# Kernel optimization log

Measured on AMD Instinct MI355X. Metric: run time of the kernel, lower is better.

The kernel has to match this reference:

```python
import jax, jax.numpy as jnp
import numpy as np

CATE_BIN = (512, 128, 256, 256, 64, 256, 256, 16, 256)
NUM_BIN = (64, 16, 128, 64, 128, 64, 512, 512)
TABLE_SIZES = CATE_BIN + NUM_BIN  # 17 tables
EMB_DIM = 16
MAX_ROWS = max(TABLE_SIZES)  # 512; tables padded/stacked for a fused gather
HIDDEN = [256, 256, 128]
OUT = 1
BATCH = 262144
BN_EPS = 1e-5


def setup_inputs() -> dict:
    key = jax.random.key(0)
    ks = jax.random.split(key, 32)
    # indices: per-column cardinality
    cols = [jax.random.randint(jax.random.fold_in(ks[0], i), (BATCH,), 0, n, dtype=jnp.int32)
            for i, n in enumerate(TABLE_SIZES)]
    x = jnp.stack(cols, axis=1)  # [B, 17] int32
    # fused/padded embedding tables: [17, MAX_ROWS, EMB_DIM]
    tables = jax.random.normal(ks[1], (len(TABLE_SIZES), MAX_ROWS, EMB_DIM), dtype=jnp.float32) * 0.05
    d_in = len(TABLE_SIZES) * EMB_DIM  # 272
    dims = [d_in] + HIDDEN
    params = {}
    for i in range(len(HIDDEN)):
        params[f"W{i}"] = jax.random.normal(ks[2 + 4 * i], (dims[i], dims[i + 1]), dtype=jnp.float32) * (1.0 / np.sqrt(dims[i]))
        params[f"b{i}"] = jnp.zeros((dims[i + 1],), dtype=jnp.float32)
        params[f"g{i}"] = jnp.ones((dims[i + 1],), dtype=jnp.float32)
        params[f"be{i}"] = jnp.zeros((dims[i + 1],), dtype=jnp.float32)
    params["Wout"] = jax.random.normal(ks[30], (HIDDEN[-1], OUT), dtype=jnp.float32) * (1.0 / np.sqrt(HIDDEN[-1]))
    params["bout"] = jnp.zeros((OUT,), dtype=jnp.float32)
    return {"x": x, "tables": tables, **params}


def _batchnorm(h, g, b):
    mu = jnp.mean(h, axis=0)
    var = jnp.var(h, axis=0)  # biased, matching torch BN forward
    return g * (h - mu) * jax.lax.rsqrt(var + BN_EPS) + b


def reference(x, tables, W0, b0, g0, be0, W1, b1, g1, be1, W2, b2, g2, be2, Wout, bout):
    # fused table-batched gather: [B, 17, 16] -> [B, 272]
    emb = tables[jnp.arange(tables.shape[0]), x]  # [B, 17, E]
    h = emb.reshape(emb.shape[0], -1)
    for W, b, g, be in ((W0, b0, g0, be0), (W1, b1, g1, be1), (W2, b2, g2, be2)):
        h = jax.nn.relu(h @ W + b)
        h = _batchnorm(h, g, be)
    return h @ Wout + bout
```

## Files before the change

### kernel.cpp

```cpp
#include <hip/hip_runtime.h>
#include <stdint.h>

#define BR 262144
#define NTAB 17
#define MAXR 512
#define DIN 272
#define AS0 296
#define ASM 264
#define NCOPY 32
#define BNEPS 1e-5f

typedef __attribute__((ext_vector_type(8))) short short8;
typedef __attribute__((ext_vector_type(4))) float f32x4;
typedef __attribute__((ext_vector_type(4))) unsigned short ushort4w;

__device__ __forceinline__ unsigned short f2bf(float f) {
  union { float f; unsigned u; } v; v.f = f;
  return (unsigned short)((v.u + 0x7FFFu + ((v.u >> 16) & 1u)) >> 16);
}
__device__ __forceinline__ float bf2f(unsigned short h) {
  union { unsigned u; float f; } v; v.u = ((unsigned)h) << 16;
  return v.f;
}

__global__ void k_prep0(const float* __restrict__ W0, const float* __restrict__ tables,
                        unsigned short* __restrict__ pW0, unsigned short* __restrict__ tb,
                        float* __restrict__ stats) {
  int tid = blockIdx.x * blockDim.x + threadIdx.x;
  int nth = gridDim.x * blockDim.x;
  for (int i = tid; i < NCOPY * 1280; i += nth) stats[i] = 0.f;
  for (int e = tid; e < 17408; e += nth) {
    const float* src = tables + (size_t)e * 8;
    f32x4 v0 = ((const f32x4*)src)[0];
    f32x4 v1 = ((const f32x4*)src)[1];
    unsigned short tmp[8];
#pragma unroll
    for (int j = 0; j < 4; j++) { tmp[j] = f2bf(v0[j]); tmp[4 + j] = f2bf(v1[j]); }
    *(short8*)&tb[(size_t)e * 8] = *(short8*)tmp;
  }
  for (int e = tid; e < 9 * 16 * 64; e += nth) {
    int l = e & 63, f = e >> 6;
    int nf = f & 15, ks = f >> 4;
    int col = nf * 16 + (l & 15);
    int kb = ks * 32 + ((l >> 4) << 3);
    unsigned short tmp[8];
#pragma unroll
    for (int j = 0; j < 8; j++) {
      int k = kb + j;
      tmp[j] = f2bf(k < DIN ? W0[k * 256 + col] : 0.f);
    }
    *(short8*)&pW0[(size_t)e * 8] = *(short8*)tmp;
  }
}

template <int KP, int NP>
__global__ void k_fold(const float* __restrict__ stats, int offSum, int offSq,
                       const float* __restrict__ g, const float* __restrict__ be,
                       const float* __restrict__ W, const float* __restrict__ b,
                       unsigned short* __restrict__ pW, float* __restrict__ bOut) {
  __shared__ float sa[KP], sc[KP];
  int tid = threadIdx.x;
  if (tid < KP) {
    float s = 0.f, q = 0.f;
    for (int c = 0; c < NCOPY; c++) {
      s += stats[c * 1280 + offSum + tid];
      q += stats[c * 1280 + offSq + tid];
    }
    float mu = s * (1.f / BR);
    float var = fmaxf(q * (1.f / BR) - mu * mu, 0.f);
    float a = g[tid] * rsqrtf(var + BNEPS);
    sa[tid] = a;
    sc[tid] = be[tid] - mu * a;
  }
  __syncthreads();
  const int NFT = NP / 16;
  const int ENT = (KP / 32) * NFT * 64;
  for (int e = blockIdx.x * blockDim.x + tid; e < ENT; e += gridDim.x * blockDim.x) {
    int l = e & 63, f = e >> 6;
    int nf = f % NFT, ks = f / NFT;
    int col = nf * 16 + (l & 15);
    int kb = ks * 32 + ((l >> 4) << 3);
    unsigned short tmp[8];
#pragma unroll
    for (int j = 0; j < 8; j++) {
      int k = kb + j;
      tmp[j] = f2bf(sa[k] * W[k * NP + col]);
    }
    *(short8*)&pW[(size_t)e * 8] = *(short8*)tmp;
  }
  if (blockIdx.x == 0 && tid < NP) {
    float s = b[tid];
    for (int k = 0; k < KP; k++) s += sc[k] * W[k * NP + tid];
    bOut[tid] = s;
  }
}

__global__ void k_foldout(const float* __restrict__ stats, int offSum, int offSq,
                          const float* __restrict__ g, const float* __restrict__ be,
                          const float* __restrict__ Wout, const float* __restrict__ bout,
                          float* __restrict__ woutp, float* __restrict__ boutp) {
  __shared__ float red[128];
  int tid = threadIdx.x;
  float s = 0.f, q = 0.f;
  for (int c = 0; c < NCOPY; c++) {
    s += stats[c * 1280 + offSum + tid];
    q += stats[c * 1280 + offSq + tid];
  }
  float mu = s * (1.f / BR);
  float var = fmaxf(q * (1.f / BR) - mu * mu, 0.f);
  float a = g[tid] * rsqrtf(var + BNEPS);
  float c = be[tid] - mu * a;
  float w = Wout[tid];
  woutp[tid] = a * w;
  red[tid] = c * w;
  __syncthreads();
  for (int st = 64; st > 0; st >>= 1) {
    if (tid < st) red[tid] += red[tid + st];
    __syncthreads();
  }
  if (tid == 0) boutp[0] = red[0] + bout[0];
}

template <int KSTEPS, int N, int AST, int MF>
__device__ __forceinline__ void gemm_body(unsigned short* As, const unsigned short* __restrict__ pW,
                                          const float* __restrict__ bias, unsigned short* __restrict__ Y,
                                          int brow, float* ssum, float* ssq,
                                          float* __restrict__ gsum, float* __restrict__ gsq) {
  const int tid = threadIdx.x;
  const int lane = tid & 63, wave = tid >> 6;
  constexpr int WC = N / 64;
  const int wc = wave % WC, wr = wave / WC;
  const int wrow = wr * (MF * 16);
  const int wcolf = wc * 4;
  const int arow = lane & 15;
  const int koff = (lane >> 4) << 3;
  const int grp = lane >> 4;

  f32x4 zero4 = {0.f, 0.f, 0.f, 0.f};
  f32x4 acc[MF][4];
#pragma unroll
  for (int mf = 0; mf < MF; mf++)
#pragma unroll
    for (int nf = 0; nf < 4; nf++) acc[mf][nf] = zero4;

  short8 bcur[4], bnxt[4];
#pragma unroll
  for (int nf = 0; nf < 4; nf++)
    bcur[nf] = *(const short8*)&pW[(size_t)((wcolf + nf) * 64 + lane) * 8];

#pragma unroll
  for (int ks = 0; ks < KSTEPS; ks++) {
    if (ks + 1 < KSTEPS) {
#pragma unroll
      for (int nf = 0; nf < 4; nf++)
        bnxt[nf] = *(const short8*)&pW[(size_t)(((ks + 1) * (N / 16) + wcolf + nf) * 64 + lane) * 8];
    }
#pragma unroll
    for (int mf = 0; mf < MF; mf++) {
      short8 am = *(const short8*)&As[(wrow + mf * 16 + arow) * AST + ks * 32 + koff];
#pragma unroll
      for (int nf = 0; nf < 4; nf++)
        acc[mf][nf] = __builtin_amdgcn_mfma_f32_16x16x32_bf16(bcur[nf], am, acc[mf][nf], 0, 0, 0);
    }
#pragma unroll
    for (int nf = 0; nf < 4; nf++) bcur[nf] = bnxt[nf];
  }

  __syncthreads();

#pragma unroll
  for (int nf = 0; nf < 4; nf++) {
    const int c0 = (wcolf + nf) * 16 + grp * 4;
    f32x4 bb = *(const f32x4*)&bias[c0];
    float s[4] = {0.f, 0.f, 0.f, 0.f}, q[4] = {0.f, 0.f, 0.f, 0.f};
#pragma unroll
    for (int mf = 0; mf < MF; mf++) {
      const int r = wrow + mf * 16 + arow;
      unsigned short o[4];
#pragma unroll
      for (int j = 0; j < 4; j++) {
        float v = fmaxf(acc[mf][nf][j] + bb[j], 0.f);
        o[j] = f2bf(v);
        s[j] += v;
        q[j] += v * v;
      }
      *(ushort4w*)&As[r * AST + c0] = *(ushort4w*)o;
    }
#pragma unroll
    for (int d = 1; d < 16; d <<= 1) {
#pragma unroll
      for (int j = 0; j < 4; j++) {
        s[j] += __shfl_xor(s[j], d, 64);
        q[j] += __shfl_xor(q[j], d, 64);
      }
    }
    if ((lane & 15) == 0) {
#pragma unroll
      for (int j = 0; j < 4; j++) {
        atomicAdd(&ssum[c0 + j], s[j]);
        atomicAdd(&ssq[c0 + j], q[j]);
      }
    }
  }
  __syncthreads();

  constexpr int CH = N / 8;
  for (int i = tid; i < 64 * CH; i += 256) {
    int row = i / CH, ch = i % CH;
    *(short8*)&Y[(size_t)(brow + row) * 256 + ch * 8] = *(const short8*)&As[row * AST + ch * 8];
  }
  if (tid < N) {
    atomicAdd(&gsum[tid], ssum[tid]);
    atomicAdd(&gsq[tid], ssq[tid]);
  }
}

__global__ __launch_bounds__(256, 3) void k_gemm0(const int* __restrict__ x, const unsigned short* __restrict__ tb,
                        const unsigned short* __restrict__ pW, const float* __restrict__ bias,
                        unsigned short* __restrict__ Y, float* __restrict__ stats, int offSum, int offSq) {
  __shared__ unsigned short As[64 * AS0];
  __shared__ int sx[64 * NTAB];
  __shared__ float ssum[256], ssq[256];
  const int tid = threadIdx.x;
  if (tid < 256) { ssum[tid] = 0.f; ssq[tid] = 0.f; }
  const int brow = blockIdx.x * 64;
  for (int t = tid; t < 64 * NTAB; t += 256) sx[t] = x[brow * NTAB + t];
  short8 z8 = {0, 0, 0, 0, 0, 0, 0, 0};
  for (int t = tid; t < 64; t += 256) {
    *(short8*)&As[t * AS0 + 272] = z8;
    *(short8*)&As[t * AS0 + 280] = z8;
    *(short8*)&As[t * AS0 + 288] = z8;
  }
  __syncthreads();
  for (int i = tid; i < 64 * NTAB * 2; i += 256) {
    int r = i / (NTAB * 2);
    int rem = i - r * (NTAB * 2);
    int tbl = rem >> 1, half = rem & 1;
    int idx = sx[r * NTAB + tbl];
    short8 v = *(const short8*)&tb[((size_t)(tbl * MAXR + idx)) * 16 + half * 8];
    *(short8*)&As[r * AS0 + tbl * 16 + half * 8] = v;
  }
  __syncthreads();
  float* gsum = stats + (size_t)(blockIdx.x & (NCOPY - 1)) * 1280 + offSum;
  float* gsq  = stats + (size_t)(blockIdx.x & (NCOPY - 1)) * 1280 + offSq;
  gemm_body<9, 256, AS0, 4>(As, pW, bias, Y, brow, ssum, ssq, gsum, gsq);
}

template <int N, int MF>
__global__ __launch_bounds__(256, 3) void k_gemm_mid(const unsigned short* __restrict__ Yin,
                           const unsigned short* __restrict__ pW, const float* __restrict__ bias,
                           unsigned short* __restrict__ Y, float* __restrict__ stats, int offSum, int offSq) {
  __shared__ unsigned short As[64 * ASM];
  __shared__ float ssum[256], ssq[256];
  const int tid = threadIdx.x;
  if (tid < 256) { ssum[tid] = 0.f; ssq[tid] = 0.f; }
  const int brow = blockIdx.x * 64;
  for (int i = tid; i < 64 * 32; i += 256) {
    int row = i >> 5, c16 = i & 31;
    short8 v = *(const short8*)&Yin[((size_t)(brow + row)) * 256 + c16 * 8];
    *(short8*)&As[row * ASM + c16 * 8] = v;
  }
  __syncthreads();
  float* gsum = stats + (size_t)(blockIdx.x & (NCOPY - 1)) * 1280 + offSum;
  float* gsq  = stats + (size_t)(blockIdx.x & (NCOPY - 1)) * 1280 + offSq;
  gemm_body<8, N, ASM, MF>(As, pW, bias, Y, brow, ssum, ssq, gsum, gsq);
}

__global__ void k_out(const unsigned short* __restrict__ Y, const float* __restrict__ woutp,
                      const float* __restrict__ boutp, float* __restrict__ out) {
  __shared__ float w[128];
  const int tid = threadIdx.x;
  if (tid < 128) w[tid] = woutp[tid];
  __syncthreads();
  const int lane = tid & 63, wave = tid >> 6;
  const int sub = lane & 7, rloc = lane >> 3;
  const int row = blockIdx.x * 32 + wave * 8 + rloc;
  const unsigned short* yr = &Y[(size_t)row * 256 + sub * 16];
  short8 v0 = *(const short8*)yr;
  short8 v1 = *(const short8*)(yr + 8);
  float acc = 0.f;
#pragma unroll
  for (int j = 0; j < 8; j++) acc += bf2f((unsigned short)v0[j]) * w[sub * 16 + j];
#pragma unroll
  for (int j = 0; j < 8; j++) acc += bf2f((unsigned short)v1[j]) * w[sub * 16 + 8 + j];
  acc += __shfl_xor(acc, 1, 64);
  acc += __shfl_xor(acc, 2, 64);
  acc += __shfl_xor(acc, 4, 64);
  if (sub == 0) out[row] = acc + boutp[0];
}

extern "C" void kernel_launch(void* const* d_in, const int* in_sizes, int n_in,
                              void* d_out, int out_size, void* d_ws, size_t ws_size,
                              hipStream_t stream) {
  const int* x = (const int*)d_in[0];
  const float* tables = (const float*)d_in[1];
  const float* W0 = (const float*)d_in[2];
  const float* b0 = (const float*)d_in[3];
  const float* g0 = (const float*)d_in[4];
  const float* be0 = (const float*)d_in[5];
  const float* W1 = (const float*)d_in[6];
  const float* b1 = (const float*)d_in[7];
  const float* g1 = (const float*)d_in[8];
  const float* be1 = (const float*)d_in[9];
  const float* W2 = (const float*)d_in[10];
  const float* b2 = (const float*)d_in[11];
  const float* g2 = (const float*)d_in[12];
  const float* be2 = (const float*)d_in[13];
  const float* Wout = (const float*)d_in[14];
  const float* bout = (const float*)d_in[15];
  float* out = (float*)d_out;

  char* ws = (char*)d_ws;
  unsigned short* Y = (unsigned short*)ws;
  size_t off = (size_t)BR * 256 * 2;
  unsigned short* pW0 = (unsigned short*)(ws + off); off += (size_t)9 * 16 * 64 * 8 * 2;
  unsigned short* pW1 = (unsigned short*)(ws + off); off += (size_t)8 * 16 * 64 * 8 * 2;
  unsigned short* pW2 = (unsigned short*)(ws + off); off += (size_t)8 * 8 * 64 * 8 * 2;
  float* b1p = (float*)(ws + off); off += 1024;
  float* b2p = (float*)(ws + off); off += 512;
  float* woutp = (float*)(ws + off); off += 512;
  float* boutp = (float*)(ws + off); off += 256;
  float* stats = (float*)(ws + off); off += (size_t)NCOPY * 1280 * 4;
  unsigned short* tb = (unsigned short*)(ws + off); off += (size_t)17 * MAXR * 16 * 2;

  const int oS0 = 0, oQ0 = 256, oS1 = 512, oQ1 = 768, oS2 = 1024, oQ2 = 1152;

  k_prep0<<<64, 256, 0, stream>>>(W0, tables, pW0, tb, stats);
  k_gemm0<<<BR / 64, 256, 0, stream>>>(x, tb, pW0, b0, Y, stats, oS0, oQ0);
  k_fold<256, 256><<<16, 256, 0, stream>>>(stats, oS0, oQ0, g0, be0, W1, b1, pW1, b1p);
  k_gemm_mid<256, 4><<<BR / 64, 256, 0, stream>>>(Y, pW1, b1p, Y, stats, oS1, oQ1);
  k_fold<256, 128><<<16, 256, 0, stream>>>(stats, oS1, oQ1, g1, be1, W2, b2, pW2, b2p);
  k_gemm_mid<128, 2><<<BR / 64, 256, 0, stream>>>(Y, pW2, b2p, Y, stats, oS2, oQ2);
  k_foldout<<<1, 128, 0, stream>>>(stats, oS2, oQ2, g2, be2, Wout, bout, woutp, boutp);
  k_out<<<BR / 32, 256, 0, stream>>>(Y, woutp, boutp, out);
}
```

Before: 251.1 us.

## Store activations in MFMA-fragment tiled layout and write epilogue directly to global

Activations move from row-major [B,256] to a per-64-row tile layout of 8-element chunks ordered by chunk then row, so the LDS A-tile matches the MFMA fragment order and loads become contiguous copies. The epilogue writes bf16 results straight to global memory and accumulates BN statistics with global atomics, dropping the LDS staging, the shared stat reduction and two barriers. A-fragment loads are double-buffered like B, stat copies go from 32 to 64, and the output kernel reads the new layout. The costs are more global atomics and scattered 8-byte global stores in the epilogue.

```diff
diff --git a/kernel.cpp b/kernel.cpp
--- a/kernel.cpp
+++ b/kernel.cpp
@@ -5,10 +5,10 @@
 #define NTAB 17
 #define MAXR 512
 #define DIN 272
-#define AS0 296
-#define ASM 264
-#define NCOPY 32
+#define NCOPY 64
 #define BNEPS 1e-5f
+
+#define TCH 32
 
 typedef __attribute__((ext_vector_type(8))) short short8;
 typedef __attribute__((ext_vector_type(4))) float f32x4;
@@ -121,11 +121,10 @@
   if (tid == 0) boutp[0] = red[0] + bout[0];
 }
 
-template <int KSTEPS, int N, int AST, int MF>
-__device__ __forceinline__ void gemm_body(unsigned short* As, const unsigned short* __restrict__ pW,
+template <int KSTEPS, int N, int MF>
+__device__ __forceinline__ void gemm_body(const unsigned short* As, const unsigned short* __restrict__ pW,
                                           const float* __restrict__ bias, unsigned short* __restrict__ Y,
-                                          int brow, float* ssum, float* ssq,
-                                          float* __restrict__ gsum, float* __restrict__ gsq) {
+                                          int tile, float* __restrict__ gsum, float* __restrict__ gsq) {
   const int tid = threadIdx.x;
   const int lane = tid & 63, wave = tid >> 6;
   constexpr int WC = N / 64;
@@ -133,7 +132,6 @@
   const int wrow = wr * (MF * 16);
   const int wcolf = wc * 4;
   const int arow = lane & 15;
-  const int koff = (lane >> 4) << 3;
   const int grp = lane >> 4;
 
   f32x4 zero4 = {0.f, 0.f, 0.f, 0.f};
@@ -143,7 +141,10 @@
 #pragma unroll
     for (int nf = 0; nf < 4; nf++) acc[mf][nf] = zero4;
 
-  short8 bcur[4], bnxt[4];
+  short8 acur[MF], anxt[MF], bcur[4], bnxt[4];
+#pragma unroll
+  for (int mf = 0; mf < MF; mf++)
+    acur[mf] = *(const short8*)&As[((0 * 4 + grp) * 64 + wrow + mf * 16 + arow) * 8];
 #pragma unroll
   for (int nf = 0; nf < 4; nf++)
     bcur[nf] = *(const short8*)&pW[(size_t)((wcolf + nf) * 64 + lane) * 8];
@@ -152,25 +153,29 @@
   for (int ks = 0; ks < KSTEPS; ks++) {
     if (ks + 1 < KSTEPS) {
 #pragma unroll
+      for (int mf = 0; mf < MF; mf++)
+        anxt[mf] = *(const short8*)&As[(((ks + 1) * 4 + grp) * 64 + wrow + mf * 16 + arow) * 8];
+#pragma unroll
       for (int nf = 0; nf < 4; nf++)
         bnxt[nf] = *(const short8*)&pW[(size_t)(((ks + 1) * (N / 16) + wcolf + nf) * 64 + lane) * 8];
     }
 #pragma unroll
-    for (int mf = 0; mf < MF; mf++) {
-      short8 am = *(const short8*)&As[(wrow + mf * 16 + arow) * AST + ks * 32 + koff];
+    for (int mf = 0; mf < MF; mf++)
 #pragma unroll
       for (int nf = 0; nf < 4; nf++)
-        acc[mf][nf] = __builtin_amdgcn_mfma_f32_16x16x32_bf16(bcur[nf], am, acc[mf][nf], 0, 0, 0);
-    }
+        acc[mf][nf] = __builtin_amdgcn_mfma_f32_16x16x32_bf16(bcur[nf], acur[mf], acc[mf][nf], 0, 0, 0);
+#pragma unroll
+    for (int mf = 0; mf < MF; mf++) acur[mf] = anxt[mf];
 #pragma unroll
     for (int nf = 0; nf < 4; nf++) bcur[nf] = bnxt[nf];
   }
 
-  __syncthreads();
-
+  const size_t tbase = (size_t)tile * TCH * 64 * 8;
 #pragma unroll
   for (int nf = 0; nf < 4; nf++) {
     const int c0 = (wcolf + nf) * 16 + grp * 4;
+    const int ch = (wcolf + nf) * 2 + (grp >> 1);
+    const int sub = (grp & 1) * 4;
     f32x4 bb = *(const f32x4*)&bias[c0];
     float s[4] = {0.f, 0.f, 0.f, 0.f}, q[4] = {0.f, 0.f, 0.f, 0.f};
 #pragma unroll
@@ -184,7 +189,7 @@
         s[j] += v;
         q[j] += v * v;
       }
-      *(ushort4w*)&As[r * AST + c0] = *(ushort4w*)o;
+      *(ushort4w*)&Y[tbase + ((size_t)ch * 64 + r) * 8 + sub] = *(ushort4w*)o;
     }
 #pragma unroll
     for (int d = 1; d < 16; d <<= 1) {
@@ -197,73 +202,54 @@
     if ((lane & 15) == 0) {
 #pragma unroll
       for (int j = 0; j < 4; j++) {
-        atomicAdd(&ssum[c0 + j], s[j]);
-        atomicAdd(&ssq[c0 + j], q[j]);
+        atomicAdd(&gsum[c0 + j], s[j]);
+        atomicAdd(&gsq[c0 + j], q[j]);
       }
     }
-  }
-  __syncthreads();
-
-  constexpr int CH = N / 8;
-  for (int i = tid; i < 64 * CH; i += 256) {
-    int row = i / CH, ch = i % CH;
-    *(short8*)&Y[(size_t)(brow + row) * 256 + ch * 8] = *(const short8*)&As[row * AST + ch * 8];
-  }
-  if (tid < N) {
-    atomicAdd(&gsum[tid], ssum[tid]);
-    atomicAdd(&gsq[tid], ssq[tid]);
   }
 }
 
 __global__ __launch_bounds__(256, 3) void k_gemm0(const int* __restrict__ x, const unsigned short* __restrict__ tb,
                         const unsigned short* __restrict__ pW, const float* __restrict__ bias,
                         unsigned short* __restrict__ Y, float* __restrict__ stats, int offSum, int offSq) {
-  __shared__ unsigned short As[64 * AS0];
+  __shared__ unsigned short As[36 * 64 * 8];
   __shared__ int sx[64 * NTAB];
-  __shared__ float ssum[256], ssq[256];
   const int tid = threadIdx.x;
-  if (tid < 256) { ssum[tid] = 0.f; ssq[tid] = 0.f; }
-  const int brow = blockIdx.x * 64;
-  for (int t = tid; t < 64 * NTAB; t += 256) sx[t] = x[brow * NTAB + t];
+  const int tile = blockIdx.x;
+  for (int t = tid; t < 64 * NTAB; t += 256) sx[t] = x[tile * 64 * NTAB + t];
   short8 z8 = {0, 0, 0, 0, 0, 0, 0, 0};
-  for (int t = tid; t < 64; t += 256) {
-    *(short8*)&As[t * AS0 + 272] = z8;
-    *(short8*)&As[t * AS0 + 280] = z8;
-    *(short8*)&As[t * AS0 + 288] = z8;
-  }
-  __syncthreads();
-  for (int i = tid; i < 64 * NTAB * 2; i += 256) {
-    int r = i / (NTAB * 2);
-    int rem = i - r * (NTAB * 2);
-    int tbl = rem >> 1, half = rem & 1;
-    int idx = sx[r * NTAB + tbl];
-    short8 v = *(const short8*)&tb[((size_t)(tbl * MAXR + idx)) * 16 + half * 8];
-    *(short8*)&As[r * AS0 + tbl * 16 + half * 8] = v;
-  }
-  __syncthreads();
-  float* gsum = stats + (size_t)(blockIdx.x & (NCOPY - 1)) * 1280 + offSum;
-  float* gsq  = stats + (size_t)(blockIdx.x & (NCOPY - 1)) * 1280 + offSq;
-  gemm_body<9, 256, AS0, 4>(As, pW, bias, Y, brow, ssum, ssq, gsum, gsq);
+  for (int i = tid; i < 128; i += 256)
+    *(short8*)&As[((34 + (i >> 6)) * 64 + (i & 63)) * 8] = z8;
+  __syncthreads();
+  for (int i = tid; i < 34 * 64; i += 256) {
+    int r = i & 63, tt = i >> 6;
+    int t = tt >> 1, half = tt & 1;
+    int idx = sx[r * NTAB + t];
+    short8 v = *(const short8*)&tb[((size_t)(t * MAXR + idx)) * 16 + half * 8];
+    *(short8*)&As[(tt * 64 + r) * 8] = v;
+  }
+  __syncthreads();
+  float* gsum = stats + (size_t)(tile & (NCOPY - 1)) * 1280 + offSum;
+  float* gsq  = stats + (size_t)(tile & (NCOPY - 1)) * 1280 + offSq;
+  gemm_body<9, 256, 4>(As, pW, bias, Y, tile, gsum, gsq);
 }
 
 template <int N, int MF>
 __global__ __launch_bounds__(256, 3) void k_gemm_mid(const unsigned short* __restrict__ Yin,
                            const unsigned short* __restrict__ pW, const float* __restrict__ bias,
                            unsigned short* __restrict__ Y, float* __restrict__ stats, int offSum, int offSq) {
-  __shared__ unsigned short As[64 * ASM];
-  __shared__ float ssum[256], ssq[256];
+  __shared__ unsigned short As[32 * 64 * 8];
   const int tid = threadIdx.x;
-  if (tid < 256) { ssum[tid] = 0.f; ssq[tid] = 0.f; }
-  const int brow = blockIdx.x * 64;
-  for (int i = tid; i < 64 * 32; i += 256) {
-    int row = i >> 5, c16 = i & 31;
-    short8 v = *(const short8*)&Yin[((size_t)(brow + row)) * 256 + c16 * 8];
-    *(short8*)&As[row * ASM + c16 * 8] = v;
-  }
-  __syncthreads();
-  float* gsum = stats + (size_t)(blockIdx.x & (NCOPY - 1)) * 1280 + offSum;
-  float* gsq  = stats + (size_t)(blockIdx.x & (NCOPY - 1)) * 1280 + offSq;
-  gemm_body<8, N, ASM, MF>(As, pW, bias, Y, brow, ssum, ssq, gsum, gsq);
+  const int tile = blockIdx.x;
+  const size_t tbase = (size_t)tile * TCH * 64 * 8;
+  for (int i = tid; i < 2048; i += 256) {
+    short8 v = *(const short8*)&Yin[tbase + (size_t)i * 8];
+    *(short8*)&As[i * 8] = v;
+  }
+  __syncthreads();
+  float* gsum = stats + (size_t)(tile & (NCOPY - 1)) * 1280 + offSum;
+  float* gsq  = stats + (size_t)(tile & (NCOPY - 1)) * 1280 + offSq;
+  gemm_body<8, N, MF>(As, pW, bias, Y, tile, gsum, gsq);
 }
 
 __global__ void k_out(const unsigned short* __restrict__ Y, const float* __restrict__ woutp,
@@ -273,20 +259,21 @@
   if (tid < 128) w[tid] = woutp[tid];
   __syncthreads();
   const int lane = tid & 63, wave = tid >> 6;
-  const int sub = lane & 7, rloc = lane >> 3;
-  const int row = blockIdx.x * 32 + wave * 8 + rloc;
-  const unsigned short* yr = &Y[(size_t)row * 256 + sub * 16];
-  short8 v0 = *(const short8*)yr;
-  short8 v1 = *(const short8*)(yr + 8);
+  const int arow = lane & 15, cpart = lane >> 4;
+  const int tile = blockIdx.x;
+  const int row = wave * 16 + arow;
+  const size_t tbase = (size_t)tile * TCH * 64 * 8;
   float acc = 0.f;
 #pragma unroll
-  for (int j = 0; j < 8; j++) acc += bf2f((unsigned short)v0[j]) * w[sub * 16 + j];
-#pragma unroll
-  for (int j = 0; j < 8; j++) acc += bf2f((unsigned short)v1[j]) * w[sub * 16 + 8 + j];
-  acc += __shfl_xor(acc, 1, 64);
-  acc += __shfl_xor(acc, 2, 64);
-  acc += __shfl_xor(acc, 4, 64);
-  if (sub == 0) out[row] = acc + boutp[0];
+  for (int i = 0; i < 4; i++) {
+    int ch = cpart * 4 + i;
+    short8 v = *(const short8*)&Y[tbase + ((size_t)ch * 64 + row) * 8];
+#pragma unroll
+    for (int j = 0; j < 8; j++) acc += bf2f((unsigned short)v[j]) * w[ch * 8 + j];
+  }
+  acc += __shfl_xor(acc, 16, 64);
+  acc += __shfl_xor(acc, 32, 64);
+  if (cpart == 0) out[tile * 64 + row] = acc + boutp[0];
 }
 
 extern "C" void kernel_launch(void* const* d_in, const int* in_sizes, int n_in,
@@ -332,5 +319,5 @@
   k_fold<256, 128><<<16, 256, 0, stream>>>(stats, oS1, oQ1, g1, be1, W2, b2, pW2, b2p);
   k_gemm_mid<128, 2><<<BR / 64, 256, 0, stream>>>(Y, pW2, b2p, Y, stats, oS2, oQ2);
   k_foldout<<<1, 128, 0, stream>>>(stats, oS2, oQ2, g2, be2, Wout, bout, woutp, boutp);
-  k_out<<<BR / 32, 256, 0, stream>>>(Y, woutp, boutp, out);
-}
+  k_out<<<BR / 64, 256, 0, stream>>>(Y, woutp, boutp, out);
+}
```

Result: slower. 282.8 us (+12.7%).
